# Performance work log

Hardware: AMD Instinct MI355X
Metric: run time of the kernel (lower is better)

Reference implementation:

```python
import jax, jax.numpy as jnp
import numpy as np

NEG_INF = -1e30  # stand-in for float('-inf') that is softmax-safe


def setup_inputs() -> dict:
    key = jax.random.key(0)
    ks = jax.random.split(key, 6)
    B, H, S, D = 2, 8, 1024, 64
    NF, K = 4, 3
    return {
        "query": jax.random.normal(ks[0], (B, H, S, D), dtype=jnp.float32),
        "keys": jax.random.normal(ks[1], (B, H, S, D), dtype=jnp.float32),
        "vals": jax.random.normal(ks[2], (B, H, S, D), dtype=jnp.float32),
        "mask": jnp.ones((B, 1, S, S), dtype=jnp.int32),
        "conv_w": jax.random.normal(ks[3], (NF, 1, K, K), dtype=jnp.float32) * (1.0 / K),
        "conv_b": jnp.zeros((NF,), dtype=jnp.float32),
        "lin_w": jax.random.normal(ks[4], (1, NF), dtype=jnp.float32) * 0.5,
        "lin_b": jnp.zeros((1,), dtype=jnp.float32),
    }


def reference(query, keys, vals, mask, conv_w, conv_b, lin_w, lin_b):
    B, H, S, D = query.shape
    NF = conv_w.shape[0]
    K = conv_w.shape[2]
    scale = jnp.asarray(D, query.dtype) ** 0.5

    # [B,H,S,S] raw dot-product scores
    dp = jnp.einsum("bhsd,bhtd->bhst", query, keys) / scale

    # conv2d over the score matrix: treat (B*H) as batch, 1 input channel
    x = dp.reshape(B * H, 1, S, S)
    conv = jax.lax.conv_general_dilated(
        x, conv_w,
        window_strides=(1, 1),
        padding=[(K // 2, K // 2), (K // 2, K // 2)],
        dimension_numbers=("NCHW", "OIHW", "NCHW"),
    ) + conv_b[None, :, None, None]
    conv = jax.nn.leaky_relu(conv, negative_slope=0.01)  # [B*H, NF, S, S]

    # per-pixel linear over the filter axis (Linear(num_filters, 1))
    conv = conv.reshape(B, H, NF, S, S)
    preattn = jnp.einsum("bhfst,f->bhst", conv, lin_w[0]) + lin_b[0]

    # masking + softmax (mask broadcasts over heads)
    preattn = jnp.where(mask == 0, jnp.asarray(NEG_INF, preattn.dtype), preattn)
    attn = jax.nn.softmax(preattn, axis=-1)

    # dropout is identity in eval mode
    return jnp.einsum("bhst,bhtd->bhsd", attn, vals)
```

## Files before the change

kernel.cpp:

```cpp
#include <hip/hip_runtime.h>
#include <math.h>

#define S_LEN 1024
#define D_DIM 64
#define NBH   16
#define RPB   14
#define NSB   74

typedef unsigned short ushort_t;
typedef unsigned int uint_t;
typedef __attribute__((ext_vector_type(8))) _Float16 half8;
typedef __attribute__((ext_vector_type(2))) _Float16 h2;
typedef __attribute__((ext_vector_type(4))) short short4v;
typedef __attribute__((ext_vector_type(4))) float f32x4;

__device__ __forceinline__ ushort_t f16bits(float x) {
    _Float16 h = (_Float16)x;
    ushort_t b;
    __builtin_memcpy(&b, &h, 2);
    return b;
}
__device__ __forceinline__ float uniform_f(float x) {
    return __int_as_float(__builtin_amdgcn_readfirstlane(__float_as_int(x)));
}
__device__ __forceinline__ float fast_exp2(float x) {
#if __has_builtin(__builtin_amdgcn_exp2f)
    return __builtin_amdgcn_exp2f(x);
#else
    return exp2f(x);
#endif
}
__device__ __forceinline__ float fmamix(int hi, uint_t xp, float w, float acc) {
    if (hi)
        asm("v_fma_mix_f32 %0, %1, %2, %0 op_sel:[1,0,0] op_sel_hi:[1,0,0]"
            : "+v"(acc) : "v"(xp), "s"(w));
    else
        asm("v_fma_mix_f32 %0, %1, %2, %0 op_sel:[0,0,0] op_sel_hi:[1,0,0]"
            : "+v"(acc) : "v"(xp), "s"(w));
    return acc;
}
__device__ __forceinline__ float fmamix3(int hi, uint_t xp, float w, float c) {
    float d;
    if (hi)
        asm("v_fma_mix_f32 %0, %1, %2, %3 op_sel:[1,0,0] op_sel_hi:[1,0,0]"
            : "=v"(d) : "v"(xp), "s"(w), "v"(c));
    else
        asm("v_fma_mix_f32 %0, %1, %2, %3 op_sel:[0,0,0] op_sel_hi:[1,0,0]"
            : "=v"(d) : "v"(xp), "s"(w), "v"(c));
    return d;
}

__global__ __launch_bounds__(256) void prep(
    const float* __restrict__ k, const float* __restrict__ v,
    const int* __restrict__ mask,
    ushort_t* __restrict__ kh, ushort_t* __restrict__ vh,
    unsigned* __restrict__ mw)
{
    __shared__ float Ls[64][65];
    const int tid = threadIdx.x;
    const int bx = blockIdx.x;
    if (bx < 512) {
        const int gid  = bx * 256 + tid;
        const int bh   = gid >> 13;
        const int tile = (gid >> 7) & 63;
        const int ch   = (gid >> 6) & 1;
        const int lane = gid & 63;
        const int quad = lane >> 4, t15 = lane & 15;
        const float* src = k + ((size_t)bh * S_LEN + tile * 16 + t15) * D_DIM
                             + ch * 32 + quad * 8;
        float x[8];
        *(float4*)(x + 0) = *(const float4*)(src);
        *(float4*)(x + 4) = *(const float4*)(src + 4);
        ushort_t hv[8];
        #pragma unroll
        for (int i = 0; i < 8; ++i) hv[i] = f16bits(x[i] * 0.125f);
        *(short4v*)(kh + (size_t)gid * 8)     = *(short4v*)(hv);
        *(short4v*)(kh + (size_t)gid * 8 + 4) = *(short4v*)(hv + 4);
    } else if (bx < 768) {
        const int bi = bx - 512;
        const int tt = bi & 15, bh = bi >> 4;
        const float* vb = v + ((size_t)bh * S_LEN + tt * 64) * D_DIM;
        #pragma unroll
        for (int p = 0; p < 4; ++p) {
            int idx = p * 1024 + tid * 4;
            int r = idx >> 6, c = idx & 63;
            float4 x = *(const float4*)(vb + r * 64 + c);
            Ls[r][c] = x.x; Ls[r][c+1] = x.y; Ls[r][c+2] = x.z; Ls[r][c+3] = x.w;
        }
        __syncthreads();
        const int d = tid >> 2, c0 = (tid & 3) * 16;
        ushort_t hi[16];
        #pragma unroll
        for (int j = 0; j < 16; ++j) hi[j] = f16bits(Ls[c0 + j][d]);
        const int tb0 = tt * 8 + (c0 >> 3);
        const size_t o0 = (((size_t)bh * 128 + tb0) * 64 + d) * 8;
        const size_t o1 = (((size_t)bh * 128 + tb0 + 1) * 64 + d) * 8;
        *(short4v*)(vh + o0)     = *(short4v*)(hi);
        *(short4v*)(vh + o0 + 4) = *(short4v*)(hi + 4);
        *(short4v*)(vh + o1)     = *(short4v*)(hi + 8);
        *(short4v*)(vh + o1 + 4) = *(short4v*)(hi + 12);
    } else {
        const int gid = (bx - 768) * 256 + tid;
        const int row = gid >> 5, wd = gid & 31;
        const int4* mp = (const int4*)(mask + (size_t)row * 1024 + wd * 32);
        unsigned bits = 0;
        #pragma unroll
        for (int p = 0; p < 8; ++p) {
            int4 qv = mp[p];
            bits |= (qv.x != 0 ? 1u : 0u) << (p * 4 + 0);
            bits |= (qv.y != 0 ? 1u : 0u) << (p * 4 + 1);
            bits |= (qv.z != 0 ? 1u : 0u) << (p * 4 + 2);
            bits |= (qv.w != 0 ? 1u : 0u) << (p * 4 + 3);
        }
        mw[(size_t)row * 32 + wd] = bits;
    }
}

#define DPSTR 1040
__global__ __launch_bounds__(512) void fused_qk_conv_av(
    const float* __restrict__ q,
    const ushort_t* __restrict__ kh, const unsigned* __restrict__ mw,
    const ushort_t* __restrict__ vh,
    const float* __restrict__ conv_w, const float* __restrict__ conv_b,
    const float* __restrict__ lin_w, const float* __restrict__ lin_b,
    float* __restrict__ out)
{
    __shared__ ushort_t dpH[16 * DPSTR];
    __shared__ float oBuf[16][68];
    __shared__ float lsRow[16];
    __shared__ unsigned mb[16][32];

    const int st = blockIdx.x, bh = blockIdx.y;
    const int s0 = st * RPB;
    const int b  = bh >> 3;
    const int tid = threadIdx.x;
    const int wave = tid >> 6, lane = tid & 63;
    const int m = lane & 15, quad = lane >> 4;

    {
        const int o = tid >> 5, wd = tid & 31;
        const int s = s0 - 1 + o;
        mb[o][wd] = (s >= 0 && s < S_LEN)
                  ? mw[((size_t)b * S_LEN + s) * 32 + wd] : 0u;
    }
    if (tid < 64) {
        const int row = tid >> 2, i = tid & 3;
        const int idx = (i < 2) ? i : 1024 + i;
        dpH[row * DPSTR + idx] = 0;
    }

    const int sA = s0 - 1 + m;
    const int sQ = sA < 0 ? 0 : (sA > S_LEN - 1 ? S_LEN - 1 : sA);
    const float* qp = q + ((size_t)bh * S_LEN + sQ) * D_DIM + quad * 8;
    float qa[16];
    *(float4*)(qa + 0)  = *(const float4*)(qp + 0);
    *(float4*)(qa + 4)  = *(const float4*)(qp + 4);
    *(float4*)(qa + 8)  = *(const float4*)(qp + 32);
    *(float4*)(qa + 12) = *(const float4*)(qp + 36);
    half8 AH0, AH1;
    #pragma unroll
    for (int i = 0; i < 8; ++i) {
        AH0[i] = (_Float16)qa[i];
        AH1[i] = (_Float16)qa[8 + i];
    }

    #pragma unroll
    for (int tt = 0; tt < 8; ++tt) {
        const int tile = wave * 8 + tt;
        const size_t kb = (((size_t)bh * 64 + tile) * 128 + lane) * 8;
        half8 KH0 = *(const half8*)(kh + kb);
        half8 KH1 = *(const half8*)(kh + kb + 512);
        f32x4 a = {0.f, 0.f, 0.f, 0.f};
        a = __builtin_amdgcn_mfma_f32_16x16x32_f16(AH0, KH0, a, 0, 0, 0);
        a = __builtin_amdgcn_mfma_f32_16x16x32_f16(AH1, KH1, a, 0, 0, 0);
        const int col = tile * 16 + m;
        #pragma unroll
        for (int r = 0; r < 4; ++r) {
            const int row = quad * 4 + r;
            const int s = s0 - 1 + row;
            const float v = (s >= 0 && s < S_LEN) ? a[r] : 0.f;
            dpH[row * DPSTR + col + 2] = f16bits(v);
        }
    }

    float w[36];
    #pragma unroll
    for (int i = 0; i < 36; ++i) w[i] = conv_w[i];
    const float L2E = 1.44269504088896341f;
    float cbV[4], aF[4], bF[4];
    #pragma unroll
    for (int f = 0; f < 4; ++f) {
        cbV[f] = conv_b[f];
        const float lwf = lin_w[f];
        aF[f] = uniform_f(0.505f * lwf * L2E);
        bF[f] = uniform_f(0.495f * lwf * L2E);
    }
    const float lbE = uniform_f(lin_b[0] * L2E);

    __syncthreads();

    const int rh = tid >> 8, cg = tid & 255, c0 = cg * 4;
    uint2 Ps[8];
    #pragma unroll
    for (int pass = 0; pass < 2; ++pass) {
        const int obase = rh * 8 + pass * 4;
        uint_t wrw[6][4];
        #pragma unroll
        for (int jj = 0; jj < 6; ++jj) {
            const int dr = obase - 1 + jj;
            if (dr >= 0 && dr < 16) {
                const ushort_t* rp = &dpH[dr * DPSTR + c0];
                const uint2 rA = *(const uint2*)rp;
                const uint2 rB = *(const uint2*)(rp + 4);
                wrw[jj][0] = rA.x; wrw[jj][1] = rA.y;
                wrw[jj][2] = rB.x; wrw[jj][3] = rB.y;
            } else {
                wrw[jj][0] = 0u; wrw[jj][1] = 0u;
                wrw[jj][2] = 0u; wrw[jj][3] = 0u;
            }
        }
        #pragma unroll
        for (int jo = 0; jo < 4; ++jo) {
            const int o = obase + jo;
            const bool act = (o >= 1) && (o <= RPB) && (s0 - 1 + o < S_LEN);
            if (act) {
                float pr[4] = {lbE, lbE, lbE, lbE};
                #pragma unroll
                for (int f = 0; f < 4; ++f) {
                    const float* wf = w + f * 9;
                    const float cbf = cbV[f];
                    float acc[4];
                    #pragma unroll
                    for (int c = 0; c < 4; ++c) {
                        const int idx = c + 1;
                        acc[c] = fmamix3(idx & 1, wrw[jo][idx >> 1],
                                         wf[0], cbf);
                    }
                    #pragma unroll
                    for (int t = 1; t < 9; ++t) {
                        const int dr = t / 3, dc = t % 3;
                        #pragma unroll
                        for (int c = 0; c < 4; ++c) {
                            const int idx = c + dc + 1;
                            acc[c] = fmamix(idx & 1, wrw[jo + dr][idx >> 1],
                                            wf[t], acc[c]);
                        }
                    }
                    const float af = aF[f], bf = bF[f];
                    #pragma unroll
                    for (int c = 0; c < 4; ++c) {
                        pr[c] = fmaf(af, acc[c], pr[c]);
                        pr[c] = fmaf(bf, fabsf(acc[c]), pr[c]);
                    }
                }
                const unsigned word = mb[o][cg >> 3];
                const unsigned nib  = (word >> ((cg & 7) * 4)) & 0xFu;
                float pv[4];
                #pragma unroll
                for (int c = 0; c < 4; ++c) {
                    const float pe = ((nib >> c) & 1u) ? pr[c] : -1e30f;
                    pv[c] = fast_exp2(pe);
                }
                Ps[pass * 4 + jo].x =
                    (uint_t)f16bits(pv[0]) | ((uint_t)f16bits(pv[1]) << 16);
                Ps[pass * 4 + jo].y =
                    (uint_t)f16bits(pv[2]) | ((uint_t)f16bits(pv[3]) << 16);
            } else {
                Ps[pass * 4 + jo].x = 0u;
                Ps[pass * 4 + jo].y = 0u;
            }
        }
    }
    __syncthreads();

    #pragma unroll
    for (int i = 0; i < 8; ++i) {
        const int o = rh * 8 + i;
        *(uint2*)&dpH[o * DPSTR + c0] = Ps[i];
    }
    __syncthreads();

    const int d0 = (wave & 3) * 16;
    const int th = wave >> 2;
    f32x4 O  = {0.f, 0.f, 0.f, 0.f};
    f32x4 RS = {0.f, 0.f, 0.f, 0.f};
    half8 ONE;
    #pragma unroll
    for (int i = 0; i < 8; ++i) ONE[i] = (_Float16)1.0f;
    const ushort_t* ph_base = &dpH[m * DPSTR + th * 512 + quad * 8];
    const ushort_t* vv_base = vh + ((size_t)bh * 65536
                                    + (size_t)(th * 64 + quad) * 512
                                    + (size_t)(d0 + m) * 8);
    #pragma unroll 4
    for (int i = 0; i < 16; ++i) {
        half8 ph = *(const half8*)(ph_base + i * 32);
        half8 vv = *(const half8*)(vv_base + (size_t)i * 2048);
        O  = __builtin_amdgcn_mfma_f32_16x16x32_f16(ph, vv, O, 0, 0, 0);
        RS = __builtin_amdgcn_mfma_f32_16x16x32_f16(ph, ONE, RS, 0, 0, 0);
    }
    if (wave < 4) {
        #pragma unroll
        for (int r = 0; r < 4; ++r) oBuf[quad * 4 + r][d0 + m] = O[r];
    }
    if (wave == 0 && m == 0) {
        #pragma unroll
        for (int r = 0; r < 4; ++r) lsRow[quad * 4 + r] = RS[r];
    }
    __syncthreads();
    if (wave >= 4) {
        #pragma unroll
        for (int r = 0; r < 4; ++r) {
            const int br = quad * 4 + r;
            const int s = s0 - 1 + br;
            if (br >= 1 && br <= RPB && s < S_LEN) {
                const float lsum = lsRow[br] + RS[r];
                out[((size_t)bh * S_LEN + s) * D_DIM + d0 + m] =
                    (O[r] + oBuf[br][d0 + m]) / lsum;
            }
        }
    }
}

extern "C" void kernel_launch(void* const* d_in, const int* in_sizes, int n_in,
                              void* d_out, int out_size, void* d_ws, size_t ws_size,
                              hipStream_t stream) {
    const float* q      = (const float*)d_in[0];
    const float* k      = (const float*)d_in[1];
    const float* v      = (const float*)d_in[2];
    const int*   mask   = (const int*)d_in[3];
    const float* conv_w = (const float*)d_in[4];
    const float* conv_b = (const float*)d_in[5];
    const float* lin_w  = (const float*)d_in[6];
    const float* lin_b  = (const float*)d_in[7];
    float* out = (float*)d_out;

    char* wsb = (char*)d_ws;
    const size_t MB = 1024 * 1024;
    ushort_t* kh = (ushort_t*)(wsb + 0 * MB);
    ushort_t* vh = (ushort_t*)(wsb + 2 * MB);
    unsigned* mw = (unsigned*)(wsb + 4 * MB);

    prep<<<dim3(1024), 256, 0, stream>>>(k, v, mask, kh, vh, mw);
    fused_qk_conv_av<<<dim3(NSB, NBH), 512, 0, stream>>>(
        q, kh, mw, vh, conv_w, conv_b, lin_w, lin_b, out);
}
```

Before: 117.9 us.

## Compute all 16 output rows per block with extra halo QK tile and swizzled LDS

Each block now produces 16 output rows instead of 14. The two halo rows needed by the 3x3 conv are computed with an extra pair of MFMAs per tile, which cuts the grid from 74 to 64 row blocks and drops the wasted edge rows in the conv and PV stages. The padded LDS stride is replaced by an XOR swizzle to avoid bank conflicts. Horizontal halo reads now fetch neighbour words with boundary checks, and the output and mask buffers are aliased into reused LDS. The trade-off is extra QK MFMA work for the halo rows and more complex indexing.

```diff
diff --git a/kernel.cpp b/kernel.cpp
--- a/kernel.cpp
+++ b/kernel.cpp
@@ -4,13 +4,13 @@
 #define S_LEN 1024
 #define D_DIM 64
 #define NBH   16
-#define RPB   14
-#define NSB   74
+#define RPB   16
+#define NSB   64
+#define DPS   1024
 
 typedef unsigned short ushort_t;
 typedef unsigned int uint_t;
 typedef __attribute__((ext_vector_type(8))) _Float16 half8;
-typedef __attribute__((ext_vector_type(2))) _Float16 h2;
 typedef __attribute__((ext_vector_type(4))) short short4v;
 typedef __attribute__((ext_vector_type(4))) float f32x4;
 
@@ -29,6 +29,11 @@
 #else
     return exp2f(x);
 #endif
+}
+__device__ __forceinline__ half8 mk8(uint2 a, uint2 b) {
+    union { uint_t u[4]; half8 h; } c;
+    c.u[0] = a.x; c.u[1] = a.y; c.u[2] = b.x; c.u[3] = b.y;
+    return c.h;
 }
 __device__ __forceinline__ float fmamix(int hi, uint_t xp, float w, float acc) {
     if (hi)
@@ -116,7 +121,6 @@
     }
 }
 
-#define DPSTR 1040
 __global__ __launch_bounds__(512) void fused_qk_conv_av(
     const float* __restrict__ q,
     const ushort_t* __restrict__ kh, const unsigned* __restrict__ mw,
@@ -125,10 +129,8 @@
     const float* __restrict__ lin_w, const float* __restrict__ lin_b,
     float* __restrict__ out)
 {
-    __shared__ ushort_t dpH[16 * DPSTR];
-    __shared__ float oBuf[16][68];
-    __shared__ float lsRow[16];
-    __shared__ unsigned mb[16][32];
+    __shared__ __align__(16) ushort_t dpH[18 * DPS];
+    __shared__ __align__(16) unsigned aux[16 * 32];
 
     const int st = blockIdx.x, bh = blockIdx.y;
     const int s0 = st * RPB;
@@ -138,19 +140,12 @@
     const int m = lane & 15, quad = lane >> 4;
 
     {
-        const int o = tid >> 5, wd = tid & 31;
-        const int s = s0 - 1 + o;
-        mb[o][wd] = (s >= 0 && s < S_LEN)
-                  ? mw[((size_t)b * S_LEN + s) * 32 + wd] : 0u;
-    }
-    if (tid < 64) {
-        const int row = tid >> 2, i = tid & 3;
-        const int idx = (i < 2) ? i : 1024 + i;
-        dpH[row * DPSTR + idx] = 0;
+        const int o1 = tid >> 5, wd = tid & 31;
+        aux[o1 * 32 + wd] = mw[((size_t)b * S_LEN + s0 + o1) * 32 + wd];
     }
 
     const int sA = s0 - 1 + m;
-    const int sQ = sA < 0 ? 0 : (sA > S_LEN - 1 ? S_LEN - 1 : sA);
+    const int sQ = sA < 0 ? 0 : sA;
     const float* qp = q + ((size_t)bh * S_LEN + sQ) * D_DIM + quad * 8;
     float qa[16];
     *(float4*)(qa + 0)  = *(const float4*)(qp + 0);
@@ -162,6 +157,20 @@
     for (int i = 0; i < 8; ++i) {
         AH0[i] = (_Float16)qa[i];
         AH1[i] = (_Float16)qa[8 + i];
+    }
+    const int sE = s0 + 15 + (m & 1);
+    const int sEc = sE > S_LEN - 1 ? S_LEN - 1 : sE;
+    const float* qp2 = q + ((size_t)bh * S_LEN + sEc) * D_DIM + quad * 8;
+    float qb[16];
+    *(float4*)(qb + 0)  = *(const float4*)(qp2 + 0);
+    *(float4*)(qb + 4)  = *(const float4*)(qp2 + 4);
+    *(float4*)(qb + 8)  = *(const float4*)(qp2 + 32);
+    *(float4*)(qb + 12) = *(const float4*)(qp2 + 36);
+    half8 AH2, AH3;
+    #pragma unroll
+    for (int i = 0; i < 8; ++i) {
+        AH2[i] = (_Float16)qb[i];
+        AH3[i] = (_Float16)qb[8 + i];
     }
 
     #pragma unroll
@@ -173,13 +182,24 @@
         f32x4 a = {0.f, 0.f, 0.f, 0.f};
         a = __builtin_amdgcn_mfma_f32_16x16x32_f16(AH0, KH0, a, 0, 0, 0);
         a = __builtin_amdgcn_mfma_f32_16x16x32_f16(AH1, KH1, a, 0, 0, 0);
+        f32x4 a2 = {0.f, 0.f, 0.f, 0.f};
+        a2 = __builtin_amdgcn_mfma_f32_16x16x32_f16(AH2, KH0, a2, 0, 0, 0);
+        a2 = __builtin_amdgcn_mfma_f32_16x16x32_f16(AH3, KH1, a2, 0, 0, 0);
         const int col = tile * 16 + m;
         #pragma unroll
         for (int r = 0; r < 4; ++r) {
             const int row = quad * 4 + r;
             const int s = s0 - 1 + row;
-            const float v = (s >= 0 && s < S_LEN) ? a[r] : 0.f;
-            dpH[row * DPSTR + col + 2] = f16bits(v);
+            const float v = (s >= 0) ? a[r] : 0.f;
+            dpH[row * DPS + (col ^ ((row & 7) << 2))] = f16bits(v);
+        }
+        if (quad == 0) {
+            #pragma unroll
+            for (int r = 0; r < 2; ++r) {
+                const int row = 16 + r;
+                const float v = (s0 + 15 + r < S_LEN) ? a2[r] : 0.f;
+                dpH[row * DPS + (col ^ ((row & 7) << 2))] = f16bits(v);
+            }
         }
     }
 
@@ -207,76 +227,70 @@
         uint_t wrw[6][4];
         #pragma unroll
         for (int jj = 0; jj < 6; ++jj) {
-            const int dr = obase - 1 + jj;
-            if (dr >= 0 && dr < 16) {
-                const ushort_t* rp = &dpH[dr * DPSTR + c0];
-                const uint2 rA = *(const uint2*)rp;
-                const uint2 rB = *(const uint2*)(rp + 4);
-                wrw[jj][0] = rA.x; wrw[jj][1] = rA.y;
-                wrw[jj][2] = rB.x; wrw[jj][3] = rB.y;
-            } else {
-                wrw[jj][0] = 0u; wrw[jj][1] = 0u;
-                wrw[jj][2] = 0u; wrw[jj][3] = 0u;
-            }
+            const int dr = obase + jj;
+            const int sw = (dr & 7) << 2;
+            const int base = dr * DPS;
+            uint_t w0 = 0u;
+            if (cg != 0)
+                w0 = ((const uint2*)&dpH[base + ((c0 - 4) ^ sw)])->y;
+            const uint2 mid = *(const uint2*)&dpH[base + (c0 ^ sw)];
+            uint_t w3 = 0u;
+            if (cg != 255)
+                w3 = *(const uint_t*)&dpH[base + ((c0 + 4) ^ sw)];
+            wrw[jj][0] = w0; wrw[jj][1] = mid.x;
+            wrw[jj][2] = mid.y; wrw[jj][3] = w3;
         }
         #pragma unroll
         for (int jo = 0; jo < 4; ++jo) {
-            const int o = obase + jo;
-            const bool act = (o >= 1) && (o <= RPB) && (s0 - 1 + o < S_LEN);
-            if (act) {
-                float pr[4] = {lbE, lbE, lbE, lbE};
+            const int o = obase + jo + 1;
+            float pr[4] = {lbE, lbE, lbE, lbE};
+            #pragma unroll
+            for (int f = 0; f < 4; ++f) {
+                const float* wf = w + f * 9;
+                const float cbf = cbV[f];
+                float acc[4];
                 #pragma unroll
-                for (int f = 0; f < 4; ++f) {
-                    const float* wf = w + f * 9;
-                    const float cbf = cbV[f];
-                    float acc[4];
+                for (int c = 0; c < 4; ++c) {
+                    const int idx = c + 1;
+                    acc[c] = fmamix3(idx & 1, wrw[jo][idx >> 1], wf[0], cbf);
+                }
+                #pragma unroll
+                for (int t = 1; t < 9; ++t) {
+                    const int dr = t / 3, dc = t % 3;
                     #pragma unroll
                     for (int c = 0; c < 4; ++c) {
-                        const int idx = c + 1;
-                        acc[c] = fmamix3(idx & 1, wrw[jo][idx >> 1],
-                                         wf[0], cbf);
-                    }
-                    #pragma unroll
-                    for (int t = 1; t < 9; ++t) {
-                        const int dr = t / 3, dc = t % 3;
-                        #pragma unroll
-                        for (int c = 0; c < 4; ++c) {
-                            const int idx = c + dc + 1;
-                            acc[c] = fmamix(idx & 1, wrw[jo + dr][idx >> 1],
-                                            wf[t], acc[c]);
-                        }
-                    }
-                    const float af = aF[f], bf = bF[f];
-                    #pragma unroll
-                    for (int c = 0; c < 4; ++c) {
-                        pr[c] = fmaf(af, acc[c], pr[c]);
-                        pr[c] = fmaf(bf, fabsf(acc[c]), pr[c]);
+                        const int idx = c + dc + 1;
+                        acc[c] = fmamix(idx & 1, wrw[jo + dr][idx >> 1],
+                                        wf[t], acc[c]);
                     }
                 }
-                const unsigned word = mb[o][cg >> 3];
-                const unsigned nib  = (word >> ((cg & 7) * 4)) & 0xFu;
-                float pv[4];
+                const float af = aF[f], bf = bF[f];
                 #pragma unroll
                 for (int c = 0; c < 4; ++c) {
-                    const float pe = ((nib >> c) & 1u) ? pr[c] : -1e30f;
-                    pv[c] = fast_exp2(pe);
+                    pr[c] = fmaf(af, acc[c], pr[c]);
+                    pr[c] = fmaf(bf, fabsf(acc[c]), pr[c]);
                 }
-                Ps[pass * 4 + jo].x =
-                    (uint_t)f16bits(pv[0]) | ((uint_t)f16bits(pv[1]) << 16);
-                Ps[pass * 4 + jo].y =
-                    (uint_t)f16bits(pv[2]) | ((uint_t)f16bits(pv[3]) << 16);
-            } else {
-                Ps[pass * 4 + jo].x = 0u;
-                Ps[pass * 4 + jo].y = 0u;
             }
+            const unsigned word = aux[(o - 1) * 32 + (cg >> 3)];
+            const unsigned nib  = (word >> ((cg & 7) * 4)) & 0xFu;
+            float pv[4];
+            #pragma unroll
+            for (int c = 0; c < 4; ++c) {
+                const float pe = ((nib >> c) & 1u) ? pr[c] : -1e30f;
+                pv[c] = fast_exp2(pe);
+            }
+            Ps[pass * 4 + jo].x =
+                (uint_t)f16bits(pv[0]) | ((uint_t)f16bits(pv[1]) << 16);
+            Ps[pass * 4 + jo].y =
+                (uint_t)f16bits(pv[2]) | ((uint_t)f16bits(pv[3]) << 16);
         }
     }
     __syncthreads();
 
     #pragma unroll
     for (int i = 0; i < 8; ++i) {
-        const int o = rh * 8 + i;
-        *(uint2*)&dpH[o * DPSTR + c0] = Ps[i];
+        const int o = rh * 8 + i + 1;
+        *(uint2*)&dpH[o * DPS + (c0 ^ ((o & 7) << 2))] = Ps[i];
     }
     __syncthreads();
 
@@ -287,38 +301,45 @@
     half8 ONE;
     #pragma unroll
     for (int i = 0; i < 8; ++i) ONE[i] = (_Float16)1.0f;
-    const ushort_t* ph_base = &dpH[m * DPSTR + th * 512 + quad * 8];
+    const int ro = m + 1;
+    const int rsw = (ro & 7) << 2;
+    const ushort_t* prow = &dpH[ro * DPS];
     const ushort_t* vv_base = vh + ((size_t)bh * 65536
                                     + (size_t)(th * 64 + quad) * 512
                                     + (size_t)(d0 + m) * 8);
     #pragma unroll 4
     for (int i = 0; i < 16; ++i) {
-        half8 ph = *(const half8*)(ph_base + i * 32);
+        const int cc = th * 512 + i * 32 + quad * 8;
+        half8 ph = mk8(*(const uint2*)&prow[cc ^ rsw],
+                       *(const uint2*)&prow[(cc + 4) ^ rsw]);
         half8 vv = *(const half8*)(vv_base + (size_t)i * 2048);
         O  = __builtin_amdgcn_mfma_f32_16x16x32_f16(ph, vv, O, 0, 0, 0);
         RS = __builtin_amdgcn_mfma_f32_16x16x32_f16(ph, ONE, RS, 0, 0, 0);
     }
+    float* const pb = (float*)dpH;
+    #define OBUF(br, d) pb[(((br) < 8) ? 0 : (17 * 512)) + ((br) & 7) * 64 \
+                           + ((d) ^ (((br) & 7) << 2))]
     if (wave < 4) {
         #pragma unroll
-        for (int r = 0; r < 4; ++r) oBuf[quad * 4 + r][d0 + m] = O[r];
+        for (int r = 0; r < 4; ++r) OBUF(quad * 4 + r, d0 + m) = O[r];
     }
     if (wave == 0 && m == 0) {
+        float* lsRow = (float*)aux;
         #pragma unroll
         for (int r = 0; r < 4; ++r) lsRow[quad * 4 + r] = RS[r];
     }
     __syncthreads();
     if (wave >= 4) {
+        const float* lsRow = (const float*)aux;
         #pragma unroll
         for (int r = 0; r < 4; ++r) {
-            const int br = quad * 4 + r;
-            const int s = s0 - 1 + br;
-            if (br >= 1 && br <= RPB && s < S_LEN) {
-                const float lsum = lsRow[br] + RS[r];
-                out[((size_t)bh * S_LEN + s) * D_DIM + d0 + m] =
-                    (O[r] + oBuf[br][d0 + m]) / lsum;
-            }
-        }
-    }
+            const int rr = quad * 4 + r;
+            const float lsum = lsRow[rr] + RS[r];
+            out[((size_t)bh * S_LEN + s0 + rr) * D_DIM + d0 + m] =
+                (O[r] + OBUF(rr, d0 + m)) / lsum;
+        }
+    }
+    #undef OBUF
 }
 
 extern "C" void kernel_launch(void* const* d_in, const int* in_sizes, int n_in,
```

Result: no change. 119.8 us (+1.6%).
